# Optimization experiments

Measured on AMD Instinct MI355X. Metric: run time of the kernel, lower is better.

The kernel has to match this reference:

```python
import jax, jax.numpy as jnp
import numpy as np

D_MODEL = 1024
N_HEADS = 16
HEAD_DIM = D_MODEL // N_HEADS
MAX_LEN = 32768
Q_LEN = 16
START_POS = MAX_LEN - Q_LEN
SCALE = 1.0 / np.sqrt(HEAD_DIM)


def setup_inputs() -> dict:
    key = jax.random.key(0)
    ks = jax.random.split(key, 7)
    xav = np.sqrt(6.0 / (D_MODEL + D_MODEL))  # xavier_uniform bound
    return {
        "query": jax.random.normal(ks[0], (Q_LEN, D_MODEL), dtype=jnp.float32),
        "Wq": jax.random.uniform(ks[1], (D_MODEL, D_MODEL), jnp.float32, -xav, xav),
        "Wk": jax.random.uniform(ks[2], (D_MODEL, D_MODEL), jnp.float32, -xav, xav),
        "Wv": jax.random.uniform(ks[3], (D_MODEL, D_MODEL), jnp.float32, -xav, xav),
        "Wo": jax.random.uniform(ks[4], (D_MODEL, D_MODEL), jnp.float32, -xav, xav),
        "cache_k": jax.random.normal(ks[5], (MAX_LEN, N_HEADS, HEAD_DIM), dtype=jnp.float32),
        "cache_v": jax.random.normal(ks[6], (MAX_LEN, N_HEADS, HEAD_DIM), dtype=jnp.float32),
        "start_pos": START_POS,
    }


def reference(query, Wq, Wk, Wv, Wo, cache_k, cache_v, start_pos):
    S = query.shape[0]
    # QKV projections (nn.Linear: y = x @ W.T), reshape to [S, H, hd]
    Q = (query @ Wq.T).reshape(S, N_HEADS, HEAD_DIM)
    K = (query @ Wk.T).reshape(S, N_HEADS, HEAD_DIM)
    V = (query @ Wv.T).reshape(S, N_HEADS, HEAD_DIM)
    # KV-cache update: write new K/V at start_pos, attend over [0, start_pos+S)
    T = start_pos + S  # cached_seq_len (static python int)
    cached_K = jax.lax.dynamic_update_slice(cache_k, K, (start_pos, 0, 0))[:T]
    cached_V = jax.lax.dynamic_update_slice(cache_v, V, (start_pos, 0, 0))[:T]
    # scores: [H, S, T]
    scores = jnp.einsum("shd,thd->hst", Q, cached_K) * jnp.float32(SCALE)
    if T > S:
        # mask key pos j > query row i + start_pos (triu with diagonal=start_pos+1)
        row = jnp.arange(S)[:, None]
        col = jnp.arange(T)[None, :]
        scores = jnp.where(col > row + start_pos, jnp.float32(-jnp.inf), scores)
    attn = jax.nn.softmax(scores, axis=-1)
    out = jnp.einsum("hst,thd->shd", attn, cached_V).reshape(S, D_MODEL)
    output = out @ Wo.T
    return output, K, V
```

## Files before the change

### kernel.cpp

```cpp
#include <hip/hip_runtime.h>

#define D      1024
#define H      16
#define HD     64
#define SQ     16
#define SP     32752
#define TT     32768
#define SCALE  0.125f
#define NC     128
#define CHUNK  256

__device__ __forceinline__ float4 ldg4(const float* p){ return *reinterpret_cast<const float4*>(p); }
__device__ __forceinline__ void   stg4(float* p, float4 v){ *reinterpret_cast<float4*>(p) = v; }

__device__ __forceinline__ float gemm16_val(const float* __restrict__ x,
                                            const float* __restrict__ W,
                                            int ochunk, int* o_out, int* li_out)
{
    const int t  = threadIdx.x;
    const int o  = ochunk * 16 + (t >> 4);
    const int ds = (t & 15) << 6;

    float4 wv[16];
    const float* wp = W + (size_t)o * D + ds;
    #pragma unroll
    for (int d4 = 0; d4 < 16; ++d4) wv[d4] = ldg4(wp + d4 * 4);

    float a[16];
    #pragma unroll
    for (int i = 0; i < 16; ++i) {
        const float* xp = x + (size_t)i * D + ds;
        float s = 0.f;
        #pragma unroll
        for (int d4 = 0; d4 < 16; ++d4) {
            float4 xv = ldg4(xp + d4 * 4);
            s += wv[d4].x * xv.x + wv[d4].y * xv.y + wv[d4].z * xv.z + wv[d4].w * xv.w;
        }
        a[i] = s;
    }
    #pragma unroll
    for (int off = 8; off >= 1; off >>= 1) {
        #pragma unroll
        for (int i = 0; i < 16; ++i) a[i] += __shfl_xor(a[i], off, 16);
    }
    const int li = t & 15;
    float v = a[0];
    #pragma unroll
    for (int i = 1; i < 16; ++i) v = (li == i) ? a[i] : v;
    *o_out = o; *li_out = li;
    return v;
}

__global__ __launch_bounds__(256) void qkv_proj(
    const float* __restrict__ q,
    const float* __restrict__ Wq, const float* __restrict__ Wk, const float* __restrict__ Wv,
    float* __restrict__ Qws, float* __restrict__ out,
    float* __restrict__ ck, float* __restrict__ cv)
{
    const int m      = blockIdx.x >> 6;
    const int ochunk = blockIdx.x & 63;
    const float* W = (m == 0) ? Wq : (m == 1) ? Wk : Wv;
    int o, li;
    float v = gemm16_val(q, W, ochunk, &o, &li);
    if (m == 0) {
        Qws[li * D + o] = v;
    } else if (m == 1) {
        out[16384 + li * D + o] = v;
        ck[(size_t)(SP + li) * D + o] = v;
    } else {
        out[32768 + li * D + o] = v;
        cv[(size_t)(SP + li) * D + o] = v;
    }
}

__global__ __launch_bounds__(256) void out_proj(
    const float* __restrict__ O, const float* __restrict__ Wo, float* __restrict__ out)
{
    int o, li;
    float v = gemm16_val(O, Wo, blockIdx.x, &o, &li);
    out[li * D + o] = v;
}

__global__ __launch_bounds__(256, 8) void attn_partial(
    const float* __restrict__ Qws, const float* __restrict__ K, const float* __restrict__ V,
    float* __restrict__ num, float* __restrict__ den)
{
    __shared__ float4 q_s[256];
    __shared__ __align__(16) float p_s[16 * CHUNK];

    const int t     = threadIdx.x;
    const int h     = blockIdx.x & 15;
    const int c     = blockIdx.x >> 4;
    const int cbase = c * CHUNK;

    {
        const int i = t >> 4, d4 = t & 15;
        q_s[t] = ldg4(Qws + (size_t)i * D + h * HD + d4 * 4);
    }
    __syncthreads();

    {
        const int j  = cbase + t;
        const float* kp = K + (size_t)j * D + h * HD;

        float s[16];
        #pragma unroll
        for (int i = 0; i < 16; ++i) s[i] = 0.f;

        #pragma unroll
        for (int d4 = 0; d4 < 16; ++d4) {
            float4 k4 = ldg4(kp + d4 * 4);
            #pragma unroll
            for (int i = 0; i < 16; ++i) {
                float4 q4 = q_s[i * 16 + d4];
                s[i] += k4.x * q4.x + k4.y * q4.y + k4.z * q4.z + k4.w * q4.w;
            }
        }
        if (j >= SP) {
            #pragma unroll
            for (int i = 0; i < 16; ++i)
                p_s[i * CHUNK + t] = (j <= SP + i) ? __expf(s[i] * SCALE) : 0.f;
        } else {
            #pragma unroll
            for (int i = 0; i < 16; ++i)
                p_s[i * CHUNK + t] = __expf(s[i] * SCALE);
        }
    }
    __syncthreads();

    {
        const int i = t >> 4, d4 = t & 15;
        const float* vp = V + (size_t)cbase * D + h * HD + d4 * 4;
        const float* pr = p_s + i * CHUNK;
        float4 o = make_float4(0.f, 0.f, 0.f, 0.f);
        float  dsum = 0.f;
        for (int j = 0; j < CHUNK; j += 8) {
            float4 pa = *reinterpret_cast<const float4*>(pr + j);
            float4 pb = *reinterpret_cast<const float4*>(pr + j + 4);
            float4 v0 = ldg4(vp + (size_t)(j + 0) * D);
            float4 v1 = ldg4(vp + (size_t)(j + 1) * D);
            float4 v2 = ldg4(vp + (size_t)(j + 2) * D);
            float4 v3 = ldg4(vp + (size_t)(j + 3) * D);
            float4 v4 = ldg4(vp + (size_t)(j + 4) * D);
            float4 v5 = ldg4(vp + (size_t)(j + 5) * D);
            float4 v6 = ldg4(vp + (size_t)(j + 6) * D);
            float4 v7 = ldg4(vp + (size_t)(j + 7) * D);
            o.x += pa.x * v0.x + pa.y * v1.x + pa.z * v2.x + pa.w * v3.x
                 + pb.x * v4.x + pb.y * v5.x + pb.z * v6.x + pb.w * v7.x;
            o.y += pa.x * v0.y + pa.y * v1.y + pa.z * v2.y + pa.w * v3.y
                 + pb.x * v4.y + pb.y * v5.y + pb.z * v6.y + pb.w * v7.y;
            o.z += pa.x * v0.z + pa.y * v1.z + pa.z * v2.z + pa.w * v3.z
                 + pb.x * v4.z + pb.y * v5.z + pb.z * v6.z + pb.w * v7.z;
            o.w += pa.x * v0.w + pa.y * v1.w + pa.z * v2.w + pa.w * v3.w
                 + pb.x * v4.w + pb.y * v5.w + pb.z * v6.w + pb.w * v7.w;
            dsum += pa.x + pa.y + pa.z + pa.w + pb.x + pb.y + pb.z + pb.w;
        }
        float* np = num + ((size_t)(h * NC + c) * 16 + i) * 64 + d4 * 4;
        stg4(np, o);
        if (d4 == 0) den[(h * NC + c) * 16 + i] = dsum;
    }
}

__global__ __launch_bounds__(256) void combine(
    const float* __restrict__ num, const float* __restrict__ den, float* __restrict__ O)
{
    const int idx = blockIdx.x * 256 + threadIdx.x;
    const int d  = idx & 63;
    const int hh = (idx >> 6) & 15;
    const int i  = idx >> 10;
    float ns = 0.f, ds = 0.f;
    #pragma unroll 8
    for (int c = 0; c < NC; ++c) {
        ns += num[((size_t)(hh * NC + c) * 16 + i) * 64 + d];
        ds += den[(hh * NC + c) * 16 + i];
    }
    O[idx] = ns / ds;
}

extern "C" void kernel_launch(void* const* d_in, const int* in_sizes, int n_in,
                              void* d_out, int out_size, void* d_ws, size_t ws_size,
                              hipStream_t stream)
{
    (void)in_sizes; (void)n_in; (void)out_size; (void)ws_size;
    const float* q  = (const float*)d_in[0];
    const float* Wq = (const float*)d_in[1];
    const float* Wk = (const float*)d_in[2];
    const float* Wv = (const float*)d_in[3];
    const float* Wo = (const float*)d_in[4];
    float* ck  = (float*)d_in[5];
    float* cv  = (float*)d_in[6];
    float* out = (float*)d_out;

    float* ws  = (float*)d_ws;
    float* Qws = ws;
    float* num = ws + 16384;
    float* den = num + (size_t)16 * NC * 16 * 64;
    float* O   = den + 16 * NC * 16;

    qkv_proj    <<<192,     256, 0, stream>>>(q, Wq, Wk, Wv, Qws, out, ck, cv);
    attn_partial<<<16 * NC, 256, 0, stream>>>(Qws, ck, cv, num, den);
    combine     <<<64,      256, 0, stream>>>(num, den, O);
    out_proj    <<<64,      256, 0, stream>>>(O, Wo, out);
}
```

Baseline: 441.2 us.

## Restructure attention partial kernel with coalesced K loads and shared-memory V tiles

Rewrites the QK phase so each 16-lane group loads one K row coalesced and reduces dot products with a transpose-style shuffle reduction, keeping Q in registers instead of shared memory. Each thread previously streamed an entire strided 256-byte K row by itself. V is now staged through a swizzled shared-memory tile in 64-row blocks, so each V row is loaded from global once per block rather than once per query row. The P buffer is padded to avoid bank conflicts. In exchange the kernel has more barriers and higher register pressure, with the occupancy hint lowered from 8 to 4.

```diff
diff --git a/kernel.cpp b/kernel.cpp
--- a/kernel.cpp
+++ b/kernel.cpp
@@ -9,6 +9,7 @@
 #define SCALE  0.125f
 #define NC     128
 #define CHUNK  256
+#define PSTR   260
 
 __device__ __forceinline__ float4 ldg4(const float* p){ return *reinterpret_cast<const float4*>(p); }
 __device__ __forceinline__ void   stg4(float* p, float4 v){ *reinterpret_cast<float4*>(p) = v; }
@@ -81,84 +82,84 @@
     out[li * D + o] = v;
 }
 
-__global__ __launch_bounds__(256, 8) void attn_partial(
+__global__ __launch_bounds__(256, 4) void attn_partial(
     const float* __restrict__ Qws, const float* __restrict__ K, const float* __restrict__ V,
     float* __restrict__ num, float* __restrict__ den)
 {
-    __shared__ float4 q_s[256];
-    __shared__ __align__(16) float p_s[16 * CHUNK];
+    __shared__ __align__(16) float p_s[16 * PSTR];
+    __shared__ __align__(16) float v_s[64 * 64];
 
     const int t     = threadIdx.x;
     const int h     = blockIdx.x & 15;
     const int c     = blockIdx.x >> 4;
     const int cbase = c * CHUNK;
-
-    {
-        const int i = t >> 4, d4 = t & 15;
-        q_s[t] = ldg4(Qws + (size_t)i * D + h * HD + d4 * 4);
+    const int w     = t >> 6;
+    const int l     = t & 63;
+    const int rr    = l >> 4;
+    const int d4    = l & 15;
+
+    float4 q4[16];
+    #pragma unroll
+    for (int i = 0; i < 16; ++i)
+        q4[i] = ldg4(Qws + (size_t)i * D + h * HD + d4 * 4);
+
+    for (int it = 0; it < 16; ++it) {
+        const int r = w * 64 + it * 4 + rr;
+        const float4 k4 = ldg4(K + (size_t)(cbase + r) * D + h * HD + d4 * 4);
+        float s[16];
+        #pragma unroll
+        for (int i = 0; i < 16; ++i)
+            s[i] = k4.x * q4[i].x + k4.y * q4[i].y + k4.z * q4[i].z + k4.w * q4[i].w;
+        #pragma unroll
+        for (int off = 8; off >= 1; off >>= 1) {
+            #pragma unroll
+            for (int i = 0; i < off; ++i) {
+                float mine = (d4 & off) ? s[i + off] : s[i];
+                float send = (d4 & off) ? s[i]       : s[i + off];
+                s[i] = mine + __shfl_xor(send, off, 16);
+            }
+        }
+        const int j = cbase + r;
+        float p = (j > SP + d4) ? 0.f : __expf(s[0] * SCALE);
+        p_s[d4 * PSTR + r] = p;
     }
     __syncthreads();
 
-    {
-        const int j  = cbase + t;
-        const float* kp = K + (size_t)j * D + h * HD;
-
-        float s[16];
-        #pragma unroll
-        for (int i = 0; i < 16; ++i) s[i] = 0.f;
-
-        #pragma unroll
-        for (int d4 = 0; d4 < 16; ++d4) {
-            float4 k4 = ldg4(kp + d4 * 4);
-            #pragma unroll
-            for (int i = 0; i < 16; ++i) {
-                float4 q4 = q_s[i * 16 + d4];
-                s[i] += k4.x * q4.x + k4.y * q4.y + k4.z * q4.z + k4.w * q4.w;
-            }
-        }
-        if (j >= SP) {
-            #pragma unroll
-            for (int i = 0; i < 16; ++i)
-                p_s[i * CHUNK + t] = (j <= SP + i) ? __expf(s[i] * SCALE) : 0.f;
-        } else {
-            #pragma unroll
-            for (int i = 0; i < 16; ++i)
-                p_s[i * CHUNK + t] = __expf(s[i] * SCALE);
-        }
-    }
-    __syncthreads();
-
-    {
-        const int i = t >> 4, d4 = t & 15;
-        const float* vp = V + (size_t)cbase * D + h * HD + d4 * 4;
-        const float* pr = p_s + i * CHUNK;
-        float4 o = make_float4(0.f, 0.f, 0.f, 0.f);
-        float  dsum = 0.f;
-        for (int j = 0; j < CHUNK; j += 8) {
-            float4 pa = *reinterpret_cast<const float4*>(pr + j);
-            float4 pb = *reinterpret_cast<const float4*>(pr + j + 4);
-            float4 v0 = ldg4(vp + (size_t)(j + 0) * D);
-            float4 v1 = ldg4(vp + (size_t)(j + 1) * D);
-            float4 v2 = ldg4(vp + (size_t)(j + 2) * D);
-            float4 v3 = ldg4(vp + (size_t)(j + 3) * D);
-            float4 v4 = ldg4(vp + (size_t)(j + 4) * D);
-            float4 v5 = ldg4(vp + (size_t)(j + 5) * D);
-            float4 v6 = ldg4(vp + (size_t)(j + 6) * D);
-            float4 v7 = ldg4(vp + (size_t)(j + 7) * D);
-            o.x += pa.x * v0.x + pa.y * v1.x + pa.z * v2.x + pa.w * v3.x
-                 + pb.x * v4.x + pb.y * v5.x + pb.z * v6.x + pb.w * v7.x;
-            o.y += pa.x * v0.y + pa.y * v1.y + pa.z * v2.y + pa.w * v3.y
-                 + pb.x * v4.y + pb.y * v5.y + pb.z * v6.y + pb.w * v7.y;
-            o.z += pa.x * v0.z + pa.y * v1.z + pa.z * v2.z + pa.w * v3.z
-                 + pb.x * v4.z + pb.y * v5.z + pb.z * v6.z + pb.w * v7.z;
-            o.w += pa.x * v0.w + pa.y * v1.w + pa.z * v2.w + pa.w * v3.w
-                 + pb.x * v4.w + pb.y * v5.w + pb.z * v6.w + pb.w * v7.w;
-            dsum += pa.x + pa.y + pa.z + pa.w + pb.x + pb.y + pb.z + pb.w;
-        }
-        float* np = num + ((size_t)(h * NC + c) * 16 + i) * 64 + d4 * 4;
-        stg4(np, o);
-        if (d4 == 0) den[(h * NC + c) * 16 + i] = dsum;
-    }
+    const int i  = t >> 4;
+    const int dq = t & 15;
+    float4 o = make_float4(0.f, 0.f, 0.f, 0.f);
+    float dsum = 0.f;
+
+    for (int sb = 0; sb < 4; ++sb) {
+        #pragma unroll
+        for (int step = 0; step < 4; ++step) {
+            const int lr = step * 16 + i;
+            const int gj = cbase + sb * 64 + lr;
+            float4 v = ldg4(V + (size_t)gj * D + h * HD + dq * 4);
+            stg4(&v_s[lr * 64 + ((dq ^ (lr & 15)) << 2)], v);
+        }
+        __syncthreads();
+
+        #pragma unroll
+        for (int rb = 0; rb < 16; ++rb) {
+            float4 p4 = *reinterpret_cast<const float4*>(&p_s[i * PSTR + sb * 64 + rb * 4]);
+            const int r0 = rb * 4;
+            float4 v0 = *reinterpret_cast<const float4*>(&v_s[(r0 + 0) * 64 + ((dq ^ ((r0 + 0) & 15)) << 2)]);
+            float4 v1 = *reinterpret_cast<const float4*>(&v_s[(r0 + 1) * 64 + ((dq ^ ((r0 + 1) & 15)) << 2)]);
+            float4 v2 = *reinterpret_cast<const float4*>(&v_s[(r0 + 2) * 64 + ((dq ^ ((r0 + 2) & 15)) << 2)]);
+            float4 v3 = *reinterpret_cast<const float4*>(&v_s[(r0 + 3) * 64 + ((dq ^ ((r0 + 3) & 15)) << 2)]);
+            o.x += p4.x * v0.x + p4.y * v1.x + p4.z * v2.x + p4.w * v3.x;
+            o.y += p4.x * v0.y + p4.y * v1.y + p4.z * v2.y + p4.w * v3.y;
+            o.z += p4.x * v0.z + p4.y * v1.z + p4.z * v2.z + p4.w * v3.z;
+            o.w += p4.x * v0.w + p4.y * v1.w + p4.z * v2.w + p4.w * v3.w;
+            dsum += p4.x + p4.y + p4.z + p4.w;
+        }
+        __syncthreads();
+    }
+
+    float* np = num + ((size_t)((h * NC + c) * 16 + i)) * 64 + dq * 4;
+    stg4(np, o);
+    if (dq == 0) den[(h * NC + c) * 16 + i] = dsum;
 }
 
 __global__ __launch_bounds__(256) void combine(
```

Result: slower. 741.7 us (+68.1%).
